# Performance work log

Measured on AMD Instinct MI355X. Metric: run time of the kernel, lower is better.

Reference implementation:

```python
import jax, jax.numpy as jnp
import numpy as np

WINDOW = 25
DIM_HEAD = 32


def _rel_pos_indices(w):
    # replicates the torch buffer: grid of (i,j) positions, pairwise offsets
    pos = np.arange(w)
    gi, gj = np.meshgrid(pos, pos, indexing='ij')
    grid = np.stack([gi.reshape(-1), gj.reshape(-1)], axis=-1)  # (w*w, 2)
    rel = grid[:, None, :] - grid[None, :, :] + (w - 1)          # (n, n, 2)
    return jnp.asarray(rel[..., 0] * (2 * w - 1) + rel[..., 1], dtype=jnp.int32)


def setup_inputs() -> dict:
    key = jax.random.key(0)
    k1, k2, k3, k4 = jax.random.split(key, 4)
    b, d, w = 32, 256, WINDOW
    heads = d // DIM_HEAD
    x = jax.random.normal(k1, (b, d, w, w), dtype=jnp.float32)
    W_qkv = jax.random.normal(k2, (d, 3 * d), dtype=jnp.float32) * 0.02
    W_out = jax.random.normal(k3, (d, d), dtype=jnp.float32) * 0.02
    rel_emb = jax.random.normal(k4, ((2 * w - 1) ** 2, heads), dtype=jnp.float32) * 0.02
    return {"x": x, "W_qkv": W_qkv, "W_out": W_out, "rel_emb": rel_emb}


def reference(x, W_qkv, W_out, rel_emb):
    b, d, H, W = x.shape
    h = d // DIM_HEAD
    scale = DIM_HEAD ** -0.5
    n = H * W

    # b d H W -> b n d
    xf = x.reshape(b, d, n).transpose(0, 2, 1)
    qkv = xf @ W_qkv                       # (b, n, 3d); columns ordered q,k,v
    q, k, v = jnp.split(qkv, 3, axis=-1)

    def to_heads(t):
        return t.reshape(b, n, h, DIM_HEAD).transpose(0, 2, 1, 3)  # b h n dh

    q = to_heads(q) * scale
    k = to_heads(k)
    v = to_heads(v)

    sim = jnp.einsum('bhid,bhjd->bhij', q, k)          # (b, h, n, n)
    bias = rel_emb[_rel_pos_indices(H)]                # (n, n, h)
    sim = sim + bias.transpose(2, 0, 1)[None]          # add per-head bias
    attn = jax.nn.softmax(sim, axis=-1)

    out = jnp.einsum('bhij,bhjd->bhid', attn, v)       # (b, h, n, dh)
    # b m (H W) dh -> b H W (m dh)  (head-major channel concat)
    out = out.transpose(0, 2, 1, 3).reshape(b, H, W, d)
    out = out @ W_out                                  # output projection (no bias)
    return out.transpose(0, 3, 1, 2)                   # b d H W
```

## Files before the change

kernel.cpp:

```cpp
#include <hip/hip_runtime.h>
#include <hip/hip_bf16.h>
#include <cstdint>

typedef __bf16 bf16x8 __attribute__((ext_vector_type(8)));
typedef __bf16 bf16x4 __attribute__((ext_vector_type(4)));
typedef float  f32x4  __attribute__((ext_vector_type(4)));
typedef float  f32x4u __attribute__((ext_vector_type(4), aligned(4)));
typedef __bf16 bf16x4u __attribute__((ext_vector_type(4), aligned(2)));
typedef unsigned short u16x4 __attribute__((ext_vector_type(4), aligned(2)));

__device__ __forceinline__ int div25(int v) { return (v * 1311) >> 15; }

#if __has_builtin(__builtin_amdgcn_exp2f)
__device__ __forceinline__ float fast_exp2(float x) { return __builtin_amdgcn_exp2f(x); }
#else
__device__ __forceinline__ float fast_exp2(float x) { return exp2f(x); }
#endif

__device__ __forceinline__ void gll16(const __bf16* g, __bf16* l)
{
    __builtin_amdgcn_global_load_lds(
        (__attribute__((address_space(1))) void*)(g),
        (__attribute__((address_space(3))) void*)(l),
        16, 0, 0);
}

__device__ __forceinline__ int sniff_isbf(const void* p)
{
    const unsigned short* x = (const unsigned short*)p;
    int cnt = 0;
    #pragma unroll
    for (int i = 0; i < 16; ++i) {
        int e = (x[2 * i] >> 7) & 0xFF;
        cnt += (e >= 90 && e <= 143) ? 1 : 0;
    }
    return cnt > 8;
}

__global__ __launch_bounds__(256) void k_pre(
    const void* __restrict__ x, const void* __restrict__ Wqkv,
    const void* __restrict__ Wout, const void* __restrict__ rel,
    __bf16* __restrict__ xT, __bf16* __restrict__ Wt, __bf16* __restrict__ WoT,
    __bf16* __restrict__ biasC)
{
    __shared__ __align__(16) float shpool[64 * 68];
    int bid = blockIdx.x;
    if (bid < 1280) {
        float (*tile)[68] = (float(*)[68])shpool;
        int isbf = sniff_isbf(x);
        int b = bid / 40, rem = bid % 40;
        int c0 = (rem % 10) * 64, r0 = (rem / 10) * 64;
        const int R = 256, C = 625;
        int t = threadIdx.x;
        int lr4 = (t >> 4) * 4;
        int lc4 = (t & 15) * 4;
        const unsigned short* sb = (const unsigned short*)x + (size_t)b * (256 * 625);
        const float*          sf = (const float*)x          + (size_t)b * (256 * 625);
        #pragma unroll
        for (int rr = 0; rr < 4; ++rr) {
            int r = r0 + lr4 + rr;
            int c = c0 + lc4;
            f32x4 v = {0.f, 0.f, 0.f, 0.f};
            if (c + 3 < C) {
                if (isbf) {
                    u16x4 u = *(const u16x4*)(sb + (size_t)r * C + c);
                    #pragma unroll
                    for (int j = 0; j < 4; ++j) v[j] = __uint_as_float((unsigned)u[j] << 16);
                } else {
                    v = *(const f32x4u*)(sf + (size_t)r * C + c);
                }
            } else {
                #pragma unroll
                for (int j = 0; j < 4; ++j) {
                    int cc2 = c + j;
                    if (cc2 < C) {
                        if (isbf) v[j] = __uint_as_float((unsigned)sb[(size_t)r * C + cc2] << 16);
                        else      v[j] = sf[(size_t)r * C + cc2];
                    }
                }
            }
            *(f32x4*)(&tile[lr4 + rr][lc4]) = v;
        }
        __syncthreads();
        __bf16* d = xT + (size_t)b * (640 * 256);
        int lc = t & 63, rc = (t >> 6) * 16;
        int c = c0 + lc;
        #pragma unroll
        for (int k = 0; k < 4; ++k) {
            bf16x4 o4;
            #pragma unroll
            for (int j = 0; j < 4; ++j) o4[j] = (__bf16)tile[rc + k * 4 + j][lc];
            *(bf16x4*)(d + (size_t)c * R + r0 + rc + k * 4) = o4;
        }
    } else if (bid < 1344) {
        float (*tile)[65] = (float(*)[65])shpool;
        int q = bid - 1280;
        int bx = q % 16, by = q / 16;
        int isbf = sniff_isbf(Wqkv);
        int isqkv = (bx < 12);
        int bxx = isqkv ? bx : (bx - 12);
        const void* src = isqkv ? Wqkv : Wout;
        __bf16* dst = isqkv ? Wt : WoT;
        int R = 256, C = isqkv ? 768 : 256;
        int r0 = by * 64, c0 = bxx * 64;
        int tc = threadIdx.x & 63, tg = threadIdx.x >> 6;
        const unsigned short* sb = (const unsigned short*)src;
        const float*          sf = (const float*)src;
        #pragma unroll
        for (int rr = 0; rr < 16; ++rr) {
            int r = r0 + tg * 16 + rr, c = c0 + tc;
            float v;
            if (isbf) v = __uint_as_float((unsigned int)sb[r * C + c] << 16);
            else      v = sf[r * C + c];
            tile[tg * 16 + rr][tc] = v;
        }
        __syncthreads();
        const float qs = 0.25503494f;
        #pragma unroll
        for (int rr = 0; rr < 16; ++rr) {
            int c = c0 + tg * 16 + rr, r = r0 + tc;
            float v = tile[tc][tg * 16 + rr];
            if (isqkv && c < 256) v *= qs;
            dst[(size_t)c * R + r] = (__bf16)v;
        }
    } else {
        const float LOG2E = 1.4426950408889634f;
        int isbf = sniff_isbf(rel);
        int q = bid - 1344;
        int ig = q % 40, h = q / 40;
        for (int t0 = 0; t0 < 10; ++t0) {
            int t  = t0 * 256 + threadIdx.x;
            int jc = t >> 7;
            int js = (t >> 6) & 1;
            int ln = t & 63;
            int qd = ln >> 4, l = ln & 15;
            int i = ig * 16 + l;
            int di = div25(i), ri = i - 25 * di;
            bf16x4 out;
            #pragma unroll
            for (int rr = 0; rr < 4; ++rr) {
                int j = jc * 32 + js * 16 + qd * 4 + rr;
                float v;
                if (j >= 625) {
                    v = -43281.f;
                } else {
                    int dj = div25(j);
                    int idx = (di - dj + 24) * 49 + ri - (j - 25 * dj) + 24;
                    idx = min(max(idx, 0), 2400);
                    float r;
                    if (isbf) r = (float)((const __bf16*)rel)[idx * 8 + h];
                    else      r = ((const float*)rel)[idx * 8 + h];
                    v = r * LOG2E;
                }
                out[rr] = (__bf16)v;
            }
            *(bf16x4*)(biasC + ((size_t)(h * 40 + ig) * 20 + jc) * 512 + ln * 8 + js * 4) = out;
        }
    }
}

#define AS(bf, r, c) pool[(size_t)(bf) * 8192 + (size_t)(r) * 32 + (c)]
#define BS(bf, r, c) pool[(size_t)(bf) * 8192 + 4096 + (size_t)(r) * 32 + (c)]
#define CS(r, c)     pool[(size_t)(r) * 44 + (c)]
__global__ __launch_bounds__(256, 2) void k_qkv(
    const __bf16* __restrict__ xT,
    const __bf16* __restrict__ Wt,
    __bf16* __restrict__ Q,
    __bf16* __restrict__ Km,
    __bf16* __restrict__ Vt)
{
    __shared__ __align__(16) __bf16 pool[16384];
    int L = blockIdx.x;
    int xcd = L & 7;
    int cc  = L >> 3;
    int pairIdx = xcd * 20 + cc / 6;
    int jt = cc - (cc / 6) * 6;
    int b  = pairIdx / 5;
    int pt = pairIdx - b * 5;
    int p0 = pt * 128, j0 = jt * 128;
    int tid = threadIdx.x;
    int w = tid >> 6, lane = tid & 63;
    int quad = lane >> 4, l15 = lane & 15;
    int wr = w >> 1, wc = w & 1;

    int srow = tid >> 2, scg = (tid & 3) * 8;
    const __bf16* ag  = xT + ((size_t)(b * 640 + p0 + srow) * 256) + scg;
    const __bf16* ag2 = ag + 64 * 256;
    const __bf16* bg  = Wt + ((size_t)(j0 + srow) * 256) + scg;
    const __bf16* bg2 = bg + 64 * 256;

    gll16(ag,  &AS(0, srow, scg));
    gll16(ag2, &AS(0, 64 + srow, scg));
    gll16(bg,  &BS(0, srow, scg));
    gll16(bg2, &BS(0, 64 + srow, scg));
    __syncthreads();

    f32x4 acc[4][4] = {};
    for (int kk = 0; kk < 8; ++kk) {
        int cur = kk & 1;
        if (kk < 7) {
            int c0 = (kk + 1) * 32;
            int nb = cur ^ 1;
            gll16(ag  + c0, &AS(nb, srow, scg));
            gll16(ag2 + c0, &AS(nb, 64 + srow, scg));
            gll16(bg  + c0, &BS(nb, srow, scg));
            gll16(bg2 + c0, &BS(nb, 64 + srow, scg));
        }
        bf16x8 af[4], bfr[4];
        #pragma unroll
        for (int t = 0; t < 4; ++t) {
            af[t]  = *(const bf16x8*)(&AS(cur, wr * 64 + t * 16 + l15, quad * 8));
            bfr[t] = *(const bf16x8*)(&BS(cur, wc * 64 + t * 16 + l15, quad * 8));
        }
        #pragma unroll
        for (int i = 0; i < 4; ++i)
            #pragma unroll
            for (int j = 0; j < 4; ++j)
                acc[i][j] = __builtin_amdgcn_mfma_f32_16x16x32_bf16(af[i], bfr[j], acc[i][j], 0, 0, 0);
        __syncthreads();
    }

    if (jt < 4) {
        for (int r = 0; r < 4; ++r) {
            __syncthreads();
            if (wc == (r >> 1)) {
                #pragma unroll
                for (int i = 0; i < 4; ++i) {
                    #pragma unroll
                    for (int js = 0; js < 2; ++js) {
                        int jp = (r & 1) * 2 + js;
                        int col = js * 16 + l15;
                        int prow = wr * 64 + i * 16 + quad * 4;
                        #pragma unroll
                        for (int rr = 0; rr < 4; ++rr)
                            CS(prow + rr, col) = (__bf16)acc[i][jp][rr];
                    }
                }
            }
            __syncthreads();
            int jj = j0 + r * 32;
            __bf16* dst; int hh;
            if (jj < 256) { hh = jj >> 5; dst = Q; }
            else          { hh = (jj - 256) >> 5; dst = Km; }
            int p = tid >> 1, d0 = (tid & 1) * 16;
            size_t base = ((size_t)((b * 8 + hh) * 640) + p0 + p) * 32 + d0;
            #pragma unroll
            for (int k4 = 0; k4 < 4; ++k4) {
                bf16x4 v4 = *(const bf16x4*)(&CS(p, d0 + k4 * 4));
                *(bf16x4*)(dst + base + k4 * 4) = v4;
            }
        }
    } else {
        #pragma unroll
        for (int i = 0; i < 4; ++i) {
            #pragma unroll
            for (int j = 0; j < 4; ++j) {
                int jj = j0 + wc * 64 + j * 16 + l15 - 512;
                int h = jj >> 5, t = jj & 31;
                int p = p0 + wr * 64 + i * 16 + quad * 4;
                bf16x4 vv;
                #pragma unroll
                for (int rr = 0; rr < 4; ++rr) vv[rr] = (__bf16)acc[i][j][rr];
                *(bf16x4*)(Vt + ((size_t)((b * 8 + h) * 32) + t) * 640 + p) = vv;
            }
        }
    }
}

__global__ __launch_bounds__(640, 2) void k_attn(
    const __bf16* __restrict__ Q,
    const __bf16* __restrict__ Km,
    const __bf16* __restrict__ Vt,
    const __bf16* __restrict__ biasC,
    __bf16* __restrict__ ctx)
{
    __shared__ __align__(16) __bf16 P[10][2][64][44];
    __shared__ float ssum[10][64];
    int bh = blockIdx.x, b = bh >> 3, h = bh & 7;
    int tid = threadIdx.x, w = tid >> 6, lane = tid & 63;
    int quad = lane >> 4, l15 = lane & 15;
    int i0 = w * 64;

    bf16x8 qa[4];
    #pragma unroll
    for (int m = 0; m < 4; ++m)
        qa[m] = *(const bf16x8*)(Q + ((size_t)bh * 640 + i0 + 16 * m + l15) * 32 + quad * 8);
    const __bf16* kbase = Km + (size_t)bh * 640 * 32 + quad * 8;
    const __bf16* vbase = Vt + ((size_t)bh * 32 + l15) * 640 + quad * 8;
    const __bf16* bcb   = biasC + (size_t)(h * 40 + (i0 >> 4)) * 10240 + lane * 8;

    f32x4 o[4][2] = {};
    float psum[4] = {0.f, 0.f, 0.f, 0.f};

    bf16x8 k0 = *(const bf16x8*)(kbase + (size_t)l15 * 32);
    bf16x8 k1 = *(const bf16x8*)(kbase + (size_t)(16 + l15) * 32);
    bf16x8 bc[4];
    #pragma unroll
    for (int m = 0; m < 4; ++m)
        bc[m] = *(const bf16x8*)(bcb + m * 10240);
    bf16x8 vC0 = {}, vC1 = {};

    for (int c = 0; c < 20; ++c) {
        int buf = c & 1;
        f32x4 s[4][2];
        __builtin_amdgcn_s_setprio(1);
        #pragma unroll
        for (int m = 0; m < 4; ++m) {
            f32x4 f0, f1;
            #pragma unroll
            for (int rr = 0; rr < 4; ++rr) { f0[rr] = (float)bc[m][rr]; f1[rr] = (float)bc[m][4 + rr]; }
            s[m][0] = __builtin_amdgcn_mfma_f32_16x16x32_bf16(k0, qa[m], f0, 0, 0, 0);
            s[m][1] = __builtin_amdgcn_mfma_f32_16x16x32_bf16(k1, qa[m], f1, 0, 0, 0);
        }
        __builtin_amdgcn_s_setprio(0);
        int cn = min(c + 1, 19);
        bf16x8 k0n = *(const bf16x8*)(kbase + (size_t)(cn * 32 + l15) * 32);
        bf16x8 k1n = *(const bf16x8*)(kbase + (size_t)(cn * 32 + 16 + l15) * 32);
        bf16x8 vN0 = *(const bf16x8*)(vbase + c * 32);
        bf16x8 vN1 = *(const bf16x8*)(vbase + (size_t)16 * 640 + c * 32);
        bf16x8 bn[4];
        #pragma unroll
        for (int m = 0; m < 4; ++m)
            bn[m] = *(const bf16x8*)(bcb + m * 10240 + cn * 512);
        bf16x4 pk[4][2];
        #pragma unroll
        for (int m = 0; m < 4; ++m) {
            #pragma unroll
            for (int rr = 0; rr < 4; ++rr) {
                float e0 = fast_exp2(s[m][0][rr]); psum[m] += e0; pk[m][0][rr] = (__bf16)e0;
                float e1 = fast_exp2(s[m][1][rr]); psum[m] += e1; pk[m][1][rr] = (__bf16)e1;
            }
        }
        if (c > 0) {
            __builtin_amdgcn_s_setprio(1);
            #pragma unroll
            for (int m = 0; m < 4; ++m) {
                bf16x8 pa = *(const bf16x8*)(&P[w][buf ^ 1][16 * m + l15][quad * 8]);
                o[m][0] = __builtin_amdgcn_mfma_f32_16x16x32_bf16(pa, vC0, o[m][0], 0, 0, 0);
                o[m][1] = __builtin_amdgcn_mfma_f32_16x16x32_bf16(pa, vC1, o[m][1], 0, 0, 0);
            }
            __builtin_amdgcn_s_setprio(0);
        }
        #pragma unroll
        for (int m = 0; m < 4; ++m) {
            *(bf16x4*)(&P[w][buf][16 * m + l15][quad * 4])      = pk[m][0];
            *(bf16x4*)(&P[w][buf][16 * m + l15][16 + quad * 4]) = pk[m][1];
        }
        k0 = k0n; k1 = k1n; vC0 = vN0; vC1 = vN1;
        #pragma unroll
        for (int m = 0; m < 4; ++m) bc[m] = bn[m];
    }
    __builtin_amdgcn_s_setprio(1);
    #pragma unroll
    for (int m = 0; m < 4; ++m) {
        bf16x8 pa = *(const bf16x8*)(&P[w][1][16 * m + l15][quad * 8]);
        o[m][0] = __builtin_amdgcn_mfma_f32_16x16x32_bf16(pa, vC0, o[m][0], 0, 0, 0);
        o[m][1] = __builtin_amdgcn_mfma_f32_16x16x32_bf16(pa, vC1, o[m][1], 0, 0, 0);
    }
    __builtin_amdgcn_s_setprio(0);

    #pragma unroll
    for (int m = 0; m < 4; ++m) {
        psum[m] += __shfl_xor(psum[m], 16);
        psum[m] += __shfl_xor(psum[m], 32);
    }
    if (quad == 0)
        #pragma unroll
        for (int m = 0; m < 4; ++m) ssum[w][16 * m + l15] = psum[m];
    #pragma unroll
    for (int m = 0; m < 4; ++m) {
        #pragma unroll
        for (int rr = 0; rr < 4; ++rr) {
            int il = 16 * m + quad * 4 + rr;
            float inv = 1.f / ssum[w][il];
            size_t base = ((size_t)b * 640 + i0 + il) * 256 + h * 32;
            ctx[base + l15]      = (__bf16)(o[m][0][rr] * inv);
            ctx[base + 16 + l15] = (__bf16)(o[m][1][rr] * inv);
        }
    }
}

__global__ __launch_bounds__(256, 2) void k_outproj(
    const __bf16* __restrict__ ctx,
    const __bf16* __restrict__ WoT,
    const void* __restrict__ xorig,
    void* __restrict__ out)
{
    __shared__ __align__(16) __bf16 pool2[20480];
    int isbf = sniff_isbf(xorig);
    int b = blockIdx.y, pt = blockIdx.x;
    int p0 = pt * 64;
    int tid = threadIdx.x, w = tid >> 6, lane = tid & 63;
    int quad = lane >> 4, l15 = lane & 15;
    int srow = tid >> 2, scg = (tid & 3) * 8;
    const __bf16* ag = ctx + ((size_t)(b * 640 + p0 + srow) * 256) + scg;
    const __bf16* bg = WoT + (size_t)srow * 256 + scg;

    gll16(ag,            &pool2[(size_t)srow * 32 + scg]);
    gll16(bg,            &pool2[2048 + (size_t)srow * 32 + scg]);
    gll16(bg + 64 * 256, &pool2[2048 + (size_t)(64 + srow) * 32 + scg]);
    gll16(bg + 128 * 256,&pool2[2048 + (size_t)(128 + srow) * 32 + scg]);
    gll16(bg + 192 * 256,&pool2[2048 + (size_t)(192 + srow) * 32 + scg]);
    __syncthreads();

    f32x4 acc[4][4] = {};
    for (int kk = 0; kk < 8; ++kk) {
        int cur = kk & 1;
        size_t base = (size_t)cur * 10240;
        if (kk < 7) {
            int c0 = (kk + 1) * 32;
            size_t nb = (size_t)(cur ^ 1) * 10240;
            gll16(ag + c0,             &pool2[nb + (size_t)srow * 32 + scg]);
            gll16(bg + c0,             &pool2[nb + 2048 + (size_t)srow * 32 + scg]);
            gll16(bg + 64 * 256 + c0,  &pool2[nb + 2048 + (size_t)(64 + srow) * 32 + scg]);
            gll16(bg + 128 * 256 + c0, &pool2[nb + 2048 + (size_t)(128 + srow) * 32 + scg]);
            gll16(bg + 192 * 256 + c0, &pool2[nb + 2048 + (size_t)(192 + srow) * 32 + scg]);
        }
        bf16x8 af[4], bfr[4];
        #pragma unroll
        for (int t = 0; t < 4; ++t) {
            af[t]  = *(const bf16x8*)(&pool2[base + (size_t)(t * 16 + l15) * 32 + quad * 8]);
            bfr[t] = *(const bf16x8*)(&pool2[base + 2048 + (size_t)(w * 64 + t * 16 + l15) * 32 + quad * 8]);
        }
        #pragma unroll
        for (int i = 0; i < 4; ++i)
            #pragma unroll
            for (int j = 0; j < 4; ++j)
                acc[i][j] = __builtin_amdgcn_mfma_f32_16x16x32_bf16(af[i], bfr[j], acc[i][j], 0, 0, 0);
        __syncthreads();
    }
    __bf16* outb = (__bf16*)out;
    float*  outf = (float*)out;
    #pragma unroll
    for (int i = 0; i < 4; ++i) {
        int p = p0 + i * 16 + quad * 4;
        #pragma unroll
        for (int j = 0; j < 4; ++j) {
            int co = w * 64 + j * 16 + l15;
            size_t o = ((size_t)(b * 256) + co) * 625 + p;
            if (p + 3 < 625) {
                if (isbf) {
                    bf16x4 v4;
                    #pragma unroll
                    for (int rr = 0; rr < 4; ++rr) v4[rr] = (__bf16)acc[i][j][rr];
                    *(bf16x4u*)(outb + o) = v4;
                } else {
                    *(f32x4u*)(outf + o) = acc[i][j];
                }
            } else {
                #pragma unroll
                for (int rr = 0; rr < 4; ++rr) {
                    if (p + rr < 625) {
                        if (isbf) outb[o + rr] = (__bf16)acc[i][j][rr];
                        else      outf[o + rr] = acc[i][j][rr];
                    }
                }
            }
        }
    }
}

extern "C" void kernel_launch(void* const* d_in, const int* in_sizes, int n_in,
                              void* d_out, int out_size, void* d_ws, size_t ws_size,
                              hipStream_t stream)
{
    const void* x    = d_in[0];
    const void* Wqkv = d_in[1];
    const void* Wout = d_in[2];
    const void* rel  = d_in[3];

    __bf16* ws    = (__bf16*)d_ws;
    __bf16* xT    = ws;
    __bf16* Wt    = xT + 10485760;
    __bf16* WoT   = Wt + 196608;
    __bf16* Q     = WoT + 65536;
    __bf16* Km    = Q + 5242880;
    __bf16* Vt    = Km + 5242880;
    __bf16* biasC = Vt + 5242880;
    __bf16* ctx   = biasC + 3276800;

    k_pre<<<1664, 256, 0, stream>>>(x, Wqkv, Wout, rel, xT, Wt, WoT, biasC);
    k_qkv<<<dim3(960), 256, 0, stream>>>(xT, Wt, Q, Km, Vt);
    k_attn<<<dim3(256), 640, 0, stream>>>(Q, Km, Vt, biasC, ctx);
    k_outproj<<<dim3(10, 32), 256, 0, stream>>>(ctx, WoT, x, d_out);
}
```

Measured before the change: 146.9 us.

## Vectorize bias build across heads and stage outproj stores through LDS

The bias-construction blocks in k_pre now process all 8 heads per block: each relative-embedding row is read as one vector load and eight head outputs are written, so that block count drops from 320 to 40. The out-projection epilogue first transposes accumulators through shared memory so each lane writes four contiguous positions per output channel, aiming for more coalesced global stores. The cost is extra LDS traffic and registers in the epilogue, and fewer, longer-running bias blocks.

```diff
diff --git a/kernel.cpp b/kernel.cpp
--- a/kernel.cpp
+++ b/kernel.cpp
@@ -126,8 +126,9 @@
     } else {
         const float LOG2E = 1.4426950408889634f;
         int isbf = sniff_isbf(rel);
-        int q = bid - 1344;
-        int ig = q % 40, h = q / 40;
+        int ig = bid - 1344;
+        const __bf16* relb = (const __bf16*)rel;
+        const float*  relf = (const float*)rel;
         for (int t0 = 0; t0 < 10; ++t0) {
             int t  = t0 * 256 + threadIdx.x;
             int jc = t >> 7;
@@ -136,25 +137,34 @@
             int qd = ln >> 4, l = ln & 15;
             int i = ig * 16 + l;
             int di = div25(i), ri = i - 25 * di;
-            bf16x4 out;
+            bf16x4 outh[8];
             #pragma unroll
             for (int rr = 0; rr < 4; ++rr) {
                 int j = jc * 32 + js * 16 + qd * 4 + rr;
-                float v;
                 if (j >= 625) {
-                    v = -43281.f;
+                    #pragma unroll
+                    for (int h = 0; h < 8; ++h) outh[h][rr] = (__bf16)(-43281.f);
                 } else {
                     int dj = div25(j);
                     int idx = (di - dj + 24) * 49 + ri - (j - 25 * dj) + 24;
                     idx = min(max(idx, 0), 2400);
-                    float r;
-                    if (isbf) r = (float)((const __bf16*)rel)[idx * 8 + h];
-                    else      r = ((const float*)rel)[idx * 8 + h];
-                    v = r * LOG2E;
+                    if (isbf) {
+                        bf16x8 r8 = *(const bf16x8*)(relb + (size_t)idx * 8);
+                        #pragma unroll
+                        for (int h = 0; h < 8; ++h) outh[h][rr] = (__bf16)((float)r8[h] * LOG2E);
+                    } else {
+                        f32x4u ra = *(const f32x4u*)(relf + (size_t)idx * 8);
+                        f32x4u rb = *(const f32x4u*)(relf + (size_t)idx * 8 + 4);
+                        #pragma unroll
+                        for (int h = 0; h < 4; ++h) outh[h][rr]     = (__bf16)(ra[h] * LOG2E);
+                        #pragma unroll
+                        for (int h = 0; h < 4; ++h) outh[4 + h][rr] = (__bf16)(rb[h] * LOG2E);
+                    }
                 }
-                out[rr] = (__bf16)v;
-            }
-            *(bf16x4*)(biasC + ((size_t)(h * 40 + ig) * 20 + jc) * 512 + ln * 8 + js * 4) = out;
+            }
+            #pragma unroll
+            for (int h = 0; h < 8; ++h)
+                *(bf16x4*)(biasC + ((size_t)(h * 40 + ig) * 20 + jc) * 512 + ln * 8 + js * 4) = outh[h];
         }
     }
 }
@@ -429,30 +439,44 @@
                 acc[i][j] = __builtin_amdgcn_mfma_f32_16x16x32_bf16(af[i], bfr[j], acc[i][j], 0, 0, 0);
         __syncthreads();
     }
+
+    float* fpool = (float*)pool2;
+    int wb = w * (32 * 68);
     __bf16* outb = (__bf16*)out;
     float*  outf = (float*)out;
     #pragma unroll
-    for (int i = 0; i < 4; ++i) {
-        int p = p0 + i * 16 + quad * 4;
-        #pragma unroll
-        for (int j = 0; j < 4; ++j) {
-            int co = w * 64 + j * 16 + l15;
+    for (int pr = 0; pr < 2; ++pr) {
+        #pragma unroll
+        for (int jp = 0; jp < 2; ++jp) {
+            int j = pr * 2 + jp;
+            int co_l = jp * 16 + l15;
+            #pragma unroll
+            for (int i = 0; i < 4; ++i)
+                *(f32x4*)(&fpool[wb + co_l * 68 + i * 16 + quad * 4]) = acc[i][j];
+        }
+        #pragma unroll
+        for (int it = 0; it < 8; ++it) {
+            int co_l = it * 4 + quad;
+            int co = w * 64 + pr * 32 + co_l;
+            int pl = l15 * 4;
+            f32x4 v = *(const f32x4*)(&fpool[wb + co_l * 68 + pl]);
+            int p = p0 + pl;
             size_t o = ((size_t)(b * 256) + co) * 625 + p;
             if (p + 3 < 625) {
                 if (isbf) {
                     bf16x4 v4;
                     #pragma unroll
-                    for (int rr = 0; rr < 4; ++rr) v4[rr] = (__bf16)acc[i][j][rr];
+                    for (int rr = 0; rr < 4; ++rr) v4[rr] = (__bf16)v[rr];
                     *(bf16x4u*)(outb + o) = v4;
                 } else {
-                    *(f32x4u*)(outf + o) = acc[i][j];
+                    *(f32x4u*)(outf + o) = v;
                 }
             } else {
                 #pragma unroll
                 for (int rr = 0; rr < 4; ++rr) {
                     if (p + rr < 625) {
-                        if (isbf) outb[o + rr] = (__bf16)acc[i][j][rr];
-                        else      outf[o + rr] = acc[i][j][rr];
+                        if (isbf) outb[o + rr] = (__bf16)v[rr];
+                        else      outf[o + rr] = v[rr];
                     }
                 }
             }
@@ -479,7 +503,7 @@
     __bf16* biasC = Vt + 5242880;
     __bf16* ctx   = biasC + 3276800;
 
-    k_pre<<<1664, 256, 0, stream>>>(x, Wqkv, Wout, rel, xT, Wt, WoT, biasC);
+    k_pre<<<1384, 256, 0, stream>>>(x, Wqkv, Wout, rel, xT, Wt, WoT, biasC);
     k_qkv<<<dim3(960), 256, 0, stream>>>(xT, Wt, Q, Km, Vt);
     k_attn<<<dim3(256), 640, 0, stream>>>(Q, Km, Vt, biasC, ctx);
     k_outproj<<<dim3(10, 32), 256, 0, stream>>>(ctx, WoT, x, d_out);
```

Result: slower. 151.7 us (+3.3%).

## Software-pipeline QK MFMA one chunk ahead of softmax in attention kernel

Applied to the files above, without the earlier changes.

Restructures the attention loop so the QK^T+bias MFMAs for the next key chunk are issued after the exp/PV work of the current chunk, with K and bias loads prefetched two chunks ahead. This is meant to overlap MFMA latency with the transcendental exp work and hide global load latency. The launch bounds drop from 2 to 1 block per CU, which allows more registers per thread for the extra live state but may lower occupancy.

```diff
diff --git a/kernel.cpp b/kernel.cpp
--- a/kernel.cpp
+++ b/kernel.cpp
@@ -267,7 +267,7 @@
     }
 }
 
-__global__ __launch_bounds__(640, 2) void k_attn(
+__global__ __launch_bounds__(640, 1) void k_attn(
     const __bf16* __restrict__ Q,
     const __bf16* __restrict__ Km,
     const __bf16* __restrict__ Vt,
@@ -298,37 +298,33 @@
     #pragma unroll
     for (int m = 0; m < 4; ++m)
         bc[m] = *(const bf16x8*)(bcb + m * 10240);
+    f32x4 sc[4][2];
+    __builtin_amdgcn_s_setprio(1);
+    #pragma unroll
+    for (int m = 0; m < 4; ++m) {
+        f32x4 f0, f1;
+        #pragma unroll
+        for (int rr = 0; rr < 4; ++rr) { f0[rr] = (float)bc[m][rr]; f1[rr] = (float)bc[m][4 + rr]; }
+        sc[m][0] = __builtin_amdgcn_mfma_f32_16x16x32_bf16(k0, qa[m], f0, 0, 0, 0);
+        sc[m][1] = __builtin_amdgcn_mfma_f32_16x16x32_bf16(k1, qa[m], f1, 0, 0, 0);
+    }
+    __builtin_amdgcn_s_setprio(0);
+    k0 = *(const bf16x8*)(kbase + (size_t)(32 + l15) * 32);
+    k1 = *(const bf16x8*)(kbase + (size_t)(48 + l15) * 32);
+    #pragma unroll
+    for (int m = 0; m < 4; ++m)
+        bc[m] = *(const bf16x8*)(bcb + m * 10240 + 512);
     bf16x8 vC0 = {}, vC1 = {};
 
     for (int c = 0; c < 20; ++c) {
         int buf = c & 1;
-        f32x4 s[4][2];
-        __builtin_amdgcn_s_setprio(1);
+        bf16x4 pk[4][2];
         #pragma unroll
         for (int m = 0; m < 4; ++m) {
-            f32x4 f0, f1;
-            #pragma unroll
-            for (int rr = 0; rr < 4; ++rr) { f0[rr] = (float)bc[m][rr]; f1[rr] = (float)bc[m][4 + rr]; }
-            s[m][0] = __builtin_amdgcn_mfma_f32_16x16x32_bf16(k0, qa[m], f0, 0, 0, 0);
-            s[m][1] = __builtin_amdgcn_mfma_f32_16x16x32_bf16(k1, qa[m], f1, 0, 0, 0);
-        }
-        __builtin_amdgcn_s_setprio(0);
-        int cn = min(c + 1, 19);
-        bf16x8 k0n = *(const bf16x8*)(kbase + (size_t)(cn * 32 + l15) * 32);
-        bf16x8 k1n = *(const bf16x8*)(kbase + (size_t)(cn * 32 + 16 + l15) * 32);
-        bf16x8 vN0 = *(const bf16x8*)(vbase + c * 32);
-        bf16x8 vN1 = *(const bf16x8*)(vbase + (size_t)16 * 640 + c * 32);
-        bf16x8 bn[4];
-        #pragma unroll
-        for (int m = 0; m < 4; ++m)
-            bn[m] = *(const bf16x8*)(bcb + m * 10240 + cn * 512);
-        bf16x4 pk[4][2];
-        #pragma unroll
-        for (int m = 0; m < 4; ++m) {
             #pragma unroll
             for (int rr = 0; rr < 4; ++rr) {
-                float e0 = fast_exp2(s[m][0][rr]); psum[m] += e0; pk[m][0][rr] = (__bf16)e0;
-                float e1 = fast_exp2(s[m][1][rr]); psum[m] += e1; pk[m][1][rr] = (__bf16)e1;
+                float e0 = fast_exp2(sc[m][0][rr]); psum[m] += e0; pk[m][0][rr] = (__bf16)e0;
+                float e1 = fast_exp2(sc[m][1][rr]); psum[m] += e1; pk[m][1][rr] = (__bf16)e1;
             }
         }
         if (c > 0) {
@@ -341,14 +337,30 @@
             }
             __builtin_amdgcn_s_setprio(0);
         }
+        __builtin_amdgcn_s_setprio(1);
+        #pragma unroll
+        for (int m = 0; m < 4; ++m) {
+            f32x4 f0, f1;
+            #pragma unroll
+            for (int rr = 0; rr < 4; ++rr) { f0[rr] = (float)bc[m][rr]; f1[rr] = (float)bc[m][4 + rr]; }
+            sc[m][0] = __builtin_amdgcn_mfma_f32_16x16x32_bf16(k0, qa[m], f0, 0, 0, 0);
+            sc[m][1] = __builtin_amdgcn_mfma_f32_16x16x32_bf16(k1, qa[m], f1, 0, 0, 0);
+        }
+        __builtin_amdgcn_s_setprio(0);
+        int c2 = min(c + 2, 19);
+        k0 = *(const bf16x8*)(kbase + (size_t)(c2 * 32 + l15) * 32);
+        k1 = *(const bf16x8*)(kbase + (size_t)(c2 * 32 + 16 + l15) * 32);
+        bf16x8 vN0 = *(const bf16x8*)(vbase + c * 32);
+        bf16x8 vN1 = *(const bf16x8*)(vbase + (size_t)16 * 640 + c * 32);
+        #pragma unroll
+        for (int m = 0; m < 4; ++m)
+            bc[m] = *(const bf16x8*)(bcb + m * 10240 + c2 * 512);
         #pragma unroll
         for (int m = 0; m < 4; ++m) {
             *(bf16x4*)(&P[w][buf][16 * m + l15][quad * 4])      = pk[m][0];
             *(bf16x4*)(&P[w][buf][16 * m + l15][16 + quad * 4]) = pk[m][1];
         }
-        k0 = k0n; k1 = k1n; vC0 = vN0; vC1 = vN1;
-        #pragma unroll
-        for (int m = 0; m < 4; ++m) bc[m] = bn[m];
+        vC0 = vN0; vC1 = vN1;
     }
     __builtin_amdgcn_s_setprio(1);
     #pragma unroll
```

Result: no change. 149.4 us (+1.7%).
